# Optimization experiments

Hardware: AMD Instinct MI355X
Metric: run time of the kernel (lower is better)

The kernel has to match this reference:

```python
import jax, jax.numpy as jnp
import numpy as np

NUM_NODES = 10000  # fixed by input spec: edge_index values in [0, 10000)


def setup_inputs() -> dict:
    key = jax.random.key(0)
    k1, k2, k3 = jax.random.split(key, 3)
    N, E, D_IN, D_OUT = NUM_NODES, 320000, 256, 256
    x = jax.random.normal(k1, (N, D_IN), dtype=jnp.float32)
    edge_index = jax.random.randint(k2, (2, E), 0, N, dtype=jnp.int64)
    # ensure node N-1 appears so num_nodes == N as in the torch code
    edge_index = edge_index.at[0, 0].set(N - 1)
    # xavier_uniform for [D_IN, D_OUT]
    limit = float(np.sqrt(6.0 / (D_IN + D_OUT)))
    weight = jax.random.uniform(k3, (D_IN, D_OUT), dtype=jnp.float32,
                                minval=-limit, maxval=limit)
    return {"x": x, "edge_index": edge_index, "weight": weight}


def _normalize_adjacency(edge_index, num_nodes):
    src, dst = edge_index[0], edge_index[1]
    ones = jnp.ones(src.shape[0], dtype=jnp.float32)
    # symmetric binarized adjacency: adj[i,j] = adj[j,i] = 1 (set, not add)
    adj = jnp.zeros((num_nodes, num_nodes), dtype=jnp.float32)
    adj = adj.at[src, dst].max(ones)
    adj = adj.at[dst, src].max(ones)
    # one round of self-loops: adj += I
    adj = adj + jnp.eye(num_nodes, dtype=jnp.float32)
    deg = jnp.sum(adj, axis=1)                    # [N]
    dinv = 1.0 / jnp.sqrt(deg)                    # [N]
    # D^-1/2 A D^-1/2 via broadcasting (equivalent to diag mms)
    return adj * dinv[:, None] * dinv[None, :]


def reference(x, edge_index, weight):
    adj = _normalize_adjacency(edge_index, NUM_NODES)  # [N, N]
    h = adj @ x                                        # [N, D_IN]
    return h @ weight                                  # [N, D_OUT]
```

## Files before the change

### kernel.cpp

```cpp
#include <hip/hip_runtime.h>
#include <hip/hip_bf16.h>
#include <stdint.h>

#define N_NODES   10000
#define D_FEAT    256
#define E_EDGES   320000
#define ROW_WORDS 313
#define ROW_STRIDE 320
#define LIST_CAP  1024

#define NB     250
#define RPB    40
#define B_CAP  8192
#define NBLK_E 313
#define NBLK_W 64

typedef __attribute__((ext_vector_type(4))) float float4v;
typedef _Float16 half8  __attribute__((ext_vector_type(8)));
typedef _Float16 half4v __attribute__((ext_vector_type(4)));

__device__ __forceinline__ uint16_t f2bf(float f) {
    union { float f; uint32_t u; } v; v.f = f;
    uint32_t r = v.u + 0x7fffu + ((v.u >> 16) & 1u);
    return (uint16_t)(r >> 16);
}
__device__ __forceinline__ float lo16(uint32_t u) {
    union { uint32_t u; float f; } v; v.u = u << 16; return v.f;
}
__device__ __forceinline__ float hi16(uint32_t u) {
    union { uint32_t u; float f; } v; v.u = u & 0xffff0000u; return v.f;
}


__global__ void __launch_bounds__(1024)
fill_buckets(const int* __restrict__ ei, uint32_t* __restrict__ bucketbuf,
             uint32_t* __restrict__ cursors,
             const float* __restrict__ w, _Float16* __restrict__ wt) {
    __shared__ uint32_t hist[256];
    __shared__ uint32_t lofs[256];
    __shared__ uint32_t base_s[256];
    __shared__ uint32_t stage[2048];
    __shared__ uint16_t sbkt[2048];
    int t = threadIdx.x;

    if (blockIdx.x >= NBLK_E) {
        int kb = (blockIdx.x - NBLK_E) * 4;
        int k = kb + (t >> 8), n = t & 255;
        float* st = (float*)stage;
        st[(n << 2) | (t >> 8)] = w[(size_t)k * D_FEAT + n];
        __syncthreads();
        if (t < 256) {
            half4v o = { (_Float16)st[t * 4 + 0], (_Float16)st[t * 4 + 1],
                         (_Float16)st[t * 4 + 2], (_Float16)st[t * 4 + 3] };
            *(half4v*)&wt[(size_t)t * D_FEAT + kb] = o;
        }
        return;
    }

    if (t < 256) hist[t] = 0;
    __syncthreads();
    int e = blockIdx.x * 1024 + t;
    int b0 = -1, b1 = -1; uint32_t ent0 = 0, ent1 = 0, s0 = 0, s1 = 0;
    if (e < E_EDGES) {
        int s = ei[e], d = ei[E_EDGES + e];
        if ((uint32_t)s < N_NODES && (uint32_t)d < N_NODES) {
            b0 = s / RPB; ent0 = ((uint32_t)(s - b0 * RPB) << 14) | (uint32_t)d;
            b1 = d / RPB; ent1 = ((uint32_t)(d - b1 * RPB) << 14) | (uint32_t)s;
            s0 = atomicAdd(&hist[b0], 1u);
            s1 = atomicAdd(&hist[b1], 1u);
        }
    }
    __syncthreads();
    if (t < 256) lofs[t] = hist[t];
    __syncthreads();
    for (int d = 1; d < 256; d <<= 1) {
        uint32_t v = 0;
        if (t < 256 && t >= d) v = lofs[t - d];
        __syncthreads();
        if (t < 256) lofs[t] += v;
        __syncthreads();
    }
    if (t < 256) base_s[t] = hist[t] ? atomicAdd(&cursors[t], hist[t]) : 0u;
    if (b0 >= 0) {
        uint32_t p0 = lofs[b0] - hist[b0] + s0;
        stage[p0] = ent0; sbkt[p0] = (uint16_t)b0;
        uint32_t p1 = lofs[b1] - hist[b1] + s1;
        stage[p1] = ent1; sbkt[p1] = (uint16_t)b1;
    }
    __syncthreads();
    uint32_t total = lofs[255];
    for (uint32_t idx = t; idx < total; idx += 1024) {
        uint32_t b = sbkt[idx];
        uint32_t pos = base_s[b] + (idx - (lofs[b] - hist[b]));
        if (pos < B_CAP) bucketbuf[(size_t)b * B_CAP + pos] = stage[idx];
    }
}

__global__ void __launch_bounds__(1024)
bucket_to_csr(const uint32_t* __restrict__ bucketbuf,
              const uint32_t* __restrict__ cursors,
              uint32_t* __restrict__ gcursor,
              uint32_t* __restrict__ col, uint32_t* __restrict__ row_base,
              uint32_t* __restrict__ row_deg, float* __restrict__ dinv,
              const float* __restrict__ x, uint16_t* __restrict__ xs) {
    __shared__ uint32_t bm[RPB * ROW_WORDS];
    __shared__ uint32_t degs[RPB];
    __shared__ uint32_t rowoff[RPB];
    __shared__ uint32_t segbase;
    int b = blockIdx.x, t = threadIdx.x;
    for (int i = t; i < RPB * ROW_WORDS; i += 1024) bm[i] = 0;
    __syncthreads();
    uint32_t cnt = min(cursors[b], (uint32_t)B_CAP);
    const uint32_t* bb = bucketbuf + (size_t)b * B_CAP;
    for (uint32_t i = t; i < cnt; i += 1024) {
        uint32_t ent = bb[i];
        uint32_t lr = ent >> 14, d = ent & 0x3FFFu;
        atomicOr(&bm[lr * ROW_WORDS + (d >> 5)], 1u << (d & 31));
    }
    __syncthreads();
    int wv = t >> 6, lane = t & 63;
    for (int r = wv; r < RPB; r += 16) {
        int pop = 0;
        #pragma unroll
        for (int k = 0; k < 5; k++) {
            int w = lane + 64 * k;
            if (w < ROW_WORDS) pop += __popc(bm[r * ROW_WORDS + w]);
        }
        #pragma unroll
        for (int off = 32; off > 0; off >>= 1) pop += __shfl_xor(pop, off, 64);
        if (lane == 0) degs[r] = (uint32_t)pop;
    }
    __syncthreads();
    if (t == 0) {
        uint32_t run = 0;
        for (int r = 0; r < RPB; r++) {
            rowoff[r] = run;
            run += (degs[r] + 3u) & ~3u;
        }
        segbase = atomicAdd(gcursor, run);
    }
    __syncthreads();
    int row0 = b * RPB;
    for (int r = wv; r < RPB; r += 16) {
        int gi = row0 + r;
        uint32_t base = segbase + rowoff[r];
        float di = 1.0f / sqrtf((float)(degs[r] + 1u));
        if (lane == 0) {
            row_base[gi] = base;
            row_deg[gi]  = degs[r];
            dinv[gi]     = di;
        }
        float4v xv = *(const float4v*)(x + (size_t)gi * D_FEAT + lane * 4);
        uint2 o;
        o.x = (uint32_t)f2bf(di * xv[0]) | ((uint32_t)f2bf(di * xv[1]) << 16);
        o.y = (uint32_t)f2bf(di * xv[2]) | ((uint32_t)f2bf(di * xv[3]) << 16);
        *(uint2*)(xs + (size_t)gi * D_FEAT + lane * 4) = o;
        uint32_t wb[5]; int tot = 0;
        #pragma unroll
        for (int k = 0; k < 5; k++) {
            int w = lane + 64 * k;
            uint32_t v = (w < ROW_WORDS) ? bm[r * ROW_WORDS + w] : 0u;
            wb[k] = v; tot += __popc(v);
        }
        int incl = tot;
        #pragma unroll
        for (int off = 1; off < 64; off <<= 1) {
            int v = __shfl_up(incl, off, 64);
            if (lane >= off) incl += v;
        }
        uint32_t p = base + (uint32_t)(incl - tot);
        #pragma unroll
        for (int k = 0; k < 5; k++) {
            uint32_t bits = wb[k];
            uint32_t cbase = (uint32_t)(lane + 64 * k) << 5;
            while (bits) {
                col[p++] = cbase + (uint32_t)__builtin_ctz(bits);
                bits &= bits - 1;
            }
        }
    }
}

__global__ void __launch_bounds__(256)
spmm_csr(const uint32_t* __restrict__ row_base, const uint32_t* __restrict__ row_deg,
         const float* __restrict__ dinv, const uint32_t* __restrict__ col,
         const uint16_t* __restrict__ xs, _Float16* __restrict__ aggh) {
    int wv = threadIdx.x >> 6, lane = threadIdx.x & 63;
    int i = blockIdx.x * 4 + wv;
    uint32_t base = row_base[i], deg = row_deg[i];
    float di = dinv[i];
    float4v z = {0.f, 0.f, 0.f, 0.f};
    float4v acc0 = z, acc1 = z, acc2 = z, acc3 = z;
    size_t ch = (size_t)lane * 4;
    uint32_t t4 = deg & ~3u;
    for (uint32_t t = 0; t < t4; t += 4) {
        uint4 jv = *(const uint4*)&col[base + t];
        uint2 g0 = *(const uint2*)(xs + (size_t)jv.x * D_FEAT + ch);
        uint2 g1 = *(const uint2*)(xs + (size_t)jv.y * D_FEAT + ch);
        uint2 g2 = *(const uint2*)(xs + (size_t)jv.z * D_FEAT + ch);
        uint2 g3 = *(const uint2*)(xs + (size_t)jv.w * D_FEAT + ch);
        acc0[0] += lo16(g0.x); acc0[1] += hi16(g0.x); acc0[2] += lo16(g0.y); acc0[3] += hi16(g0.y);
        acc1[0] += lo16(g1.x); acc1[1] += hi16(g1.x); acc1[2] += lo16(g1.y); acc1[3] += hi16(g1.y);
        acc2[0] += lo16(g2.x); acc2[1] += hi16(g2.x); acc2[2] += lo16(g2.y); acc2[3] += hi16(g2.y);
        acc3[0] += lo16(g3.x); acc3[1] += hi16(g3.x); acc3[2] += lo16(g3.y); acc3[3] += hi16(g3.y);
    }
    for (uint32_t t = t4; t < deg; t++) {
        uint32_t j = col[base + t];
        uint2 g = *(const uint2*)(xs + (size_t)j * D_FEAT + ch);
        acc0[0] += lo16(g.x); acc0[1] += hi16(g.x); acc0[2] += lo16(g.y); acc0[3] += hi16(g.y);
    }
    uint2 gs = *(const uint2*)(xs + (size_t)i * D_FEAT + ch);
    acc1[0] += lo16(gs.x); acc1[1] += hi16(gs.x); acc1[2] += lo16(gs.y); acc1[3] += hi16(gs.y);
    float4v acc = (acc0 + acc1) + (acc2 + acc3);
    half4v o = { (_Float16)(di * acc[0]), (_Float16)(di * acc[1]),
                 (_Float16)(di * acc[2]), (_Float16)(di * acc[3]) };
    *(half4v*)(aggh + (size_t)i * D_FEAT + ch) = o;
}

__global__ void __launch_bounds__(256)
gemm_mfma(const _Float16* __restrict__ aggh, const _Float16* __restrict__ wt,
          float* __restrict__ out) {
    int t = threadIdx.x;
    int wv = t >> 6, lane = t & 63;
    int quad = lane >> 4, r = lane & 15;
    int bx = blockIdx.x;
    int ct = blockIdx.y * 4 + wv;

    const _Float16* pa = aggh + (size_t)(bx * 16 + r) * D_FEAT + quad * 8;
    const _Float16* pb = wt   + (size_t)(ct * 16 + r) * D_FEAT + quad * 8;

    float4v acc = {0.f, 0.f, 0.f, 0.f};
    #pragma unroll
    for (int kk = 0; kk < D_FEAT; kk += 32) {
        half8 a = *(const half8*)(pa + kk);
        half8 b = *(const half8*)(pb + kk);
        acc = __builtin_amdgcn_mfma_f32_16x16x32_f16(a, b, acc, 0, 0, 0);
    }
    int mbase = bx * 16 + quad * 4;
    int colg  = ct * 16 + r;
    #pragma unroll
    for (int u = 0; u < 4; u++)
        out[(size_t)(mbase + u) * D_FEAT + colg] = acc[u];
}


__global__ void scatter_edges_fb(const int* __restrict__ ei,
                                 uint32_t* __restrict__ bitmap) {
    int e = blockIdx.x * blockDim.x + threadIdx.x;
    if (e >= E_EDGES) return;
    int s = ei[e], d = ei[E_EDGES + e];
    if ((uint32_t)s >= N_NODES || (uint32_t)d >= N_NODES) return;
    atomicOr(&bitmap[(size_t)s * ROW_STRIDE + (d >> 5)], 1u << (d & 31));
    atomicOr(&bitmap[(size_t)d * ROW_STRIDE + (s >> 5)], 1u << (s & 31));
}

__global__ void __launch_bounds__(256)
popc_dinv(const uint32_t* __restrict__ bitmap, float* __restrict__ dinv) {
    int wv = threadIdx.x >> 6, lane = threadIdx.x & 63;
    int i = blockIdx.x * 4 + wv;
    const uint32_t* rb = bitmap + (size_t)i * ROW_STRIDE;
    int pop = 0;
    #pragma unroll
    for (int k = 0; k < 5; k++) {
        int w = lane + 64 * k;
        if (w < ROW_WORDS) pop += __popc(rb[w]);
    }
    #pragma unroll
    for (int off = 32; off > 0; off >>= 1) pop += __shfl_xor(pop, off, 64);
    if (lane == 0) dinv[i] = 1.0f / sqrtf((float)(pop + 1));
}

__global__ void __launch_bounds__(256)
spmm_bitmap_fb(const uint32_t* __restrict__ bitmap, const float* __restrict__ dinv,
               const float* __restrict__ xf, float* __restrict__ agg) {
    __shared__ __align__(16) uint32_t lists[4][LIST_CAP];
    int wv = threadIdx.x >> 6, lane = threadIdx.x & 63;
    int i = blockIdx.x * 4 + wv;
    uint32_t* list = lists[wv];
    const uint32_t* rb = bitmap + (size_t)i * ROW_STRIDE;

    uint32_t wbits[5]; int tot = 0;
    #pragma unroll
    for (int k = 0; k < 5; k++) {
        int w = lane + 64 * k;
        uint32_t b = (w < ROW_WORDS) ? rb[w] : 0u;
        wbits[k] = b;
        tot += __popc(b);
    }
    int incl = tot;
    #pragma unroll
    for (int off = 1; off < 64; off <<= 1) {
        int v = __shfl_up(incl, off, 64);
        if (lane >= off) incl += v;
    }
    uint32_t p = (uint32_t)(incl - tot);
    uint32_t deg = (uint32_t)__shfl(incl, 63, 64);
    #pragma unroll
    for (int k = 0; k < 5; k++) {
        uint32_t bits = wbits[k];
        uint32_t base = (uint32_t)(lane + 64 * k) << 5;
        while (bits) {
            if (p < LIST_CAP) list[p] = base + (uint32_t)__builtin_ctz(bits);
            p++;
            bits &= bits - 1;
        }
    }
    if (deg > LIST_CAP) deg = LIST_CAP;

    float di = dinv[i];
    float4v z = {0.f, 0.f, 0.f, 0.f};
    float4v acc0 = z, acc1 = z, acc2 = z, acc3 = z;
    float4v sv = *(const float4v*)(xf + (size_t)i * D_FEAT + lane * 4);
    uint32_t t4 = deg & ~3u;
    for (uint32_t k = 0; k < t4; k += 4) {
        uint4 jv = *(const uint4*)&list[k];
        float d0 = dinv[jv.x], d1 = dinv[jv.y], d2 = dinv[jv.z], d3 = dinv[jv.w];
        float4v v0 = *(const float4v*)(xf + (size_t)jv.x * D_FEAT + lane * 4);
        float4v v1 = *(const float4v*)(xf + (size_t)jv.y * D_FEAT + lane * 4);
        float4v v2 = *(const float4v*)(xf + (size_t)jv.z * D_FEAT + lane * 4);
        float4v v3 = *(const float4v*)(xf + (size_t)jv.w * D_FEAT + lane * 4);
        acc0 += d0 * v0; acc1 += d1 * v1; acc2 += d2 * v2; acc3 += d3 * v3;
    }
    for (uint32_t k = t4; k < deg; k++) {
        uint32_t j = list[k];
        acc0 += dinv[j] * (*(const float4v*)(xf + (size_t)j * D_FEAT + lane * 4));
    }
    float4v acc = (acc0 + acc1) + (acc2 + acc3) + di * sv;
    *(float4v*)(agg + (size_t)i * D_FEAT + lane * 4) = di * acc;
}

__global__ void __launch_bounds__(256)
gemm_valu(float* __restrict__ io, const float* __restrict__ wf) {
    __shared__ __align__(16) float a_lds[16 * D_FEAT];
    int c = threadIdx.x;
    int r0 = blockIdx.x * 16;
    for (int idx = c; idx < 16 * D_FEAT; idx += 256)
        a_lds[idx] = io[(size_t)r0 * D_FEAT + idx];
    __syncthreads();
    float acc[16];
    #pragma unroll
    for (int r = 0; r < 16; r++) acc[r] = 0.f;
    for (int k0 = 0; k0 < D_FEAT; k0 += 4) {
        float w0 = wf[(size_t)(k0 + 0) * D_FEAT + c];
        float w1 = wf[(size_t)(k0 + 1) * D_FEAT + c];
        float w2 = wf[(size_t)(k0 + 2) * D_FEAT + c];
        float w3 = wf[(size_t)(k0 + 3) * D_FEAT + c];
        #pragma unroll
        for (int r = 0; r < 16; r++) {
            float4v av = *(const float4v*)&a_lds[r * D_FEAT + k0];
            acc[r] = fmaf(av[3], w3, fmaf(av[2], w2,
                     fmaf(av[1], w1, fmaf(av[0], w0, acc[r]))));
        }
    }
    #pragma unroll
    for (int r = 0; r < 16; r++)
        io[(size_t)(r0 + r) * D_FEAT + c] = acc[r];
}

extern "C" void kernel_launch(void* const* d_in, const int* in_sizes, int n_in,
                              void* d_out, int out_size, void* d_ws, size_t ws_size,
                              hipStream_t stream) {
    const float* x  = (const float*)d_in[0];
    const int*   ei = (const int*)d_in[1];
    const float* w  = (const float*)d_in[2];
    float* out = (float*)d_out;
    uint8_t* ws = (uint8_t*)d_ws;

    const size_t CUR_OFF  = 8192000;
    const size_t RB_OFF   = 8194048;
    const size_t RD_OFF   = 8234048;
    const size_t DI_OFF   = 8274048;
    const size_t XS_OFF   = 8314048;
    const size_t COL_OFF  = 13434048;
    const size_t WT_OFF   = 16154048;
    const size_t NEED_NEW = 16285120;
    const size_t NEED_FB  = 12840000;

    if (ws_size >= NEED_NEW) {
        uint32_t* bucketbuf = (uint32_t*)ws;
        _Float16* aggh      = (_Float16*)ws;
        uint32_t* cursors   = (uint32_t*)(ws + CUR_OFF);
        uint32_t* row_base  = (uint32_t*)(ws + RB_OFF);
        uint32_t* row_deg   = (uint32_t*)(ws + RD_OFF);
        float*    dinv      = (float*)(ws + DI_OFF);
        uint16_t* xs        = (uint16_t*)(ws + XS_OFF);
        uint32_t* col       = (uint32_t*)(ws + COL_OFF);
        _Float16* wt        = (_Float16*)(ws + WT_OFF);

        hipMemsetAsync(cursors, 0, 2048, stream);
        fill_buckets <<<NBLK_E + NBLK_W, 1024, 0, stream>>>(ei, bucketbuf, cursors, w, wt);
        bucket_to_csr<<<NB, 1024, 0, stream>>>(bucketbuf, cursors, &cursors[NB],
                                               col, row_base, row_deg, dinv, x, xs);
        spmm_csr     <<<N_NODES / 4, 256, 0, stream>>>(row_base, row_deg, dinv, col, xs, aggh);
        gemm_mfma    <<<dim3(N_NODES / 16, 4), 256, 0, stream>>>(aggh, wt, out);
    } else if (ws_size >= NEED_FB) {
        uint32_t* bitmap = (uint32_t*)ws;
        float*    dinv   = (float*)(ws + 12800000);

        hipMemsetAsync(bitmap, 0, 12800000, stream);
        scatter_edges_fb<<<(E_EDGES + 255) / 256, 256, 0, stream>>>(ei, bitmap);
        popc_dinv      <<<N_NODES / 4, 256, 0, stream>>>(bitmap, dinv);
        spmm_bitmap_fb <<<N_NODES / 4, 256, 0, stream>>>(bitmap, dinv, x, out);
        gemm_valu      <<<N_NODES / 16, 256, 0, stream>>>(out, w);
    }
}
```

Before: 142.7 us.

## Split CSR build blocks, unroll SpMM gathers to 8, stage GEMM A tile in LDS

Three separate changes. The bucket-to-CSR kernel now launches two blocks per bucket, each handling half the rows, which doubles parallelism and halves the shared bitmap size, at the cost of every block reading the full bucket and filtering it. The SpMM inner loop is unrolled to 8 neighbour gathers with 8 accumulators, putting more loads in flight. The GEMM now has one block per 16-row strip load the A tile into padded LDS once and loop over 4 column tiles per wave, which cuts redundant global reads of A but gives the GEMM 4x fewer blocks.

```diff
diff --git a/kernel.cpp b/kernel.cpp
--- a/kernel.cpp
+++ b/kernel.cpp
@@ -14,6 +14,9 @@
 #define B_CAP  8192
 #define NBLK_E 313
 #define NBLK_W 64
+#define RPC    20
+
+#define LDSTR 264
 
 typedef __attribute__((ext_vector_type(4))) float float4v;
 typedef _Float16 half8  __attribute__((ext_vector_type(8)));
@@ -103,23 +106,28 @@
               uint32_t* __restrict__ col, uint32_t* __restrict__ row_base,
               uint32_t* __restrict__ row_deg, float* __restrict__ dinv,
               const float* __restrict__ x, uint16_t* __restrict__ xs) {
-    __shared__ uint32_t bm[RPB * ROW_WORDS];
-    __shared__ uint32_t degs[RPB];
-    __shared__ uint32_t rowoff[RPB];
+    __shared__ uint32_t bm[RPC * ROW_WORDS];
+    __shared__ uint32_t degs[RPC];
+    __shared__ uint32_t rowoff[RPC];
     __shared__ uint32_t segbase;
-    int b = blockIdx.x, t = threadIdx.x;
-    for (int i = t; i < RPB * ROW_WORDS; i += 1024) bm[i] = 0;
+    int blk = blockIdx.x, t = threadIdx.x;
+    int b   = blk >> 1;
+    int lr0 = (blk & 1) * RPC;
+    for (int i = t; i < RPC * ROW_WORDS; i += 1024) bm[i] = 0;
     __syncthreads();
     uint32_t cnt = min(cursors[b], (uint32_t)B_CAP);
     const uint32_t* bb = bucketbuf + (size_t)b * B_CAP;
     for (uint32_t i = t; i < cnt; i += 1024) {
         uint32_t ent = bb[i];
-        uint32_t lr = ent >> 14, d = ent & 0x3FFFu;
-        atomicOr(&bm[lr * ROW_WORDS + (d >> 5)], 1u << (d & 31));
+        uint32_t lr = (ent >> 14) - (uint32_t)lr0;
+        if (lr < RPC) {
+            uint32_t d = ent & 0x3FFFu;
+            atomicOr(&bm[lr * ROW_WORDS + (d >> 5)], 1u << (d & 31));
+        }
     }
     __syncthreads();
     int wv = t >> 6, lane = t & 63;
-    for (int r = wv; r < RPB; r += 16) {
+    for (int r = wv; r < RPC; r += 16) {
         int pop = 0;
         #pragma unroll
         for (int k = 0; k < 5; k++) {
@@ -133,15 +141,15 @@
     __syncthreads();
     if (t == 0) {
         uint32_t run = 0;
-        for (int r = 0; r < RPB; r++) {
+        for (int r = 0; r < RPC; r++) {
             rowoff[r] = run;
             run += (degs[r] + 3u) & ~3u;
         }
         segbase = atomicAdd(gcursor, run);
     }
     __syncthreads();
-    int row0 = b * RPB;
-    for (int r = wv; r < RPB; r += 16) {
+    int row0 = b * RPB + lr0;
+    for (int r = wv; r < RPC; r += 16) {
         int gi = row0 + r;
         uint32_t base = segbase + rowoff[r];
         float di = 1.0f / sqrtf((float)(degs[r] + 1u));
@@ -190,28 +198,38 @@
     uint32_t base = row_base[i], deg = row_deg[i];
     float di = dinv[i];
     float4v z = {0.f, 0.f, 0.f, 0.f};
-    float4v acc0 = z, acc1 = z, acc2 = z, acc3 = z;
+    float4v a0 = z, a1 = z, a2 = z, a3 = z, a4 = z, a5 = z, a6 = z, a7 = z;
     size_t ch = (size_t)lane * 4;
-    uint32_t t4 = deg & ~3u;
-    for (uint32_t t = 0; t < t4; t += 4) {
-        uint4 jv = *(const uint4*)&col[base + t];
-        uint2 g0 = *(const uint2*)(xs + (size_t)jv.x * D_FEAT + ch);
-        uint2 g1 = *(const uint2*)(xs + (size_t)jv.y * D_FEAT + ch);
-        uint2 g2 = *(const uint2*)(xs + (size_t)jv.z * D_FEAT + ch);
-        uint2 g3 = *(const uint2*)(xs + (size_t)jv.w * D_FEAT + ch);
-        acc0[0] += lo16(g0.x); acc0[1] += hi16(g0.x); acc0[2] += lo16(g0.y); acc0[3] += hi16(g0.y);
-        acc1[0] += lo16(g1.x); acc1[1] += hi16(g1.x); acc1[2] += lo16(g1.y); acc1[3] += hi16(g1.y);
-        acc2[0] += lo16(g2.x); acc2[1] += hi16(g2.x); acc2[2] += lo16(g2.y); acc2[3] += hi16(g2.y);
-        acc3[0] += lo16(g3.x); acc3[1] += hi16(g3.x); acc3[2] += lo16(g3.y); acc3[3] += hi16(g3.y);
-    }
-    for (uint32_t t = t4; t < deg; t++) {
+    uint32_t t8 = deg & ~7u;
+    uint32_t t = 0;
+    for (; t < t8; t += 8) {
+        uint4 jva = *(const uint4*)&col[base + t];
+        uint4 jvb = *(const uint4*)&col[base + t + 4];
+        uint2 g0 = *(const uint2*)(xs + (size_t)jva.x * D_FEAT + ch);
+        uint2 g1 = *(const uint2*)(xs + (size_t)jva.y * D_FEAT + ch);
+        uint2 g2 = *(const uint2*)(xs + (size_t)jva.z * D_FEAT + ch);
+        uint2 g3 = *(const uint2*)(xs + (size_t)jva.w * D_FEAT + ch);
+        uint2 g4 = *(const uint2*)(xs + (size_t)jvb.x * D_FEAT + ch);
+        uint2 g5 = *(const uint2*)(xs + (size_t)jvb.y * D_FEAT + ch);
+        uint2 g6 = *(const uint2*)(xs + (size_t)jvb.z * D_FEAT + ch);
+        uint2 g7 = *(const uint2*)(xs + (size_t)jvb.w * D_FEAT + ch);
+        a0[0] += lo16(g0.x); a0[1] += hi16(g0.x); a0[2] += lo16(g0.y); a0[3] += hi16(g0.y);
+        a1[0] += lo16(g1.x); a1[1] += hi16(g1.x); a1[2] += lo16(g1.y); a1[3] += hi16(g1.y);
+        a2[0] += lo16(g2.x); a2[1] += hi16(g2.x); a2[2] += lo16(g2.y); a2[3] += hi16(g2.y);
+        a3[0] += lo16(g3.x); a3[1] += hi16(g3.x); a3[2] += lo16(g3.y); a3[3] += hi16(g3.y);
+        a4[0] += lo16(g4.x); a4[1] += hi16(g4.x); a4[2] += lo16(g4.y); a4[3] += hi16(g4.y);
+        a5[0] += lo16(g5.x); a5[1] += hi16(g5.x); a5[2] += lo16(g5.y); a5[3] += hi16(g5.y);
+        a6[0] += lo16(g6.x); a6[1] += hi16(g6.x); a6[2] += lo16(g6.y); a6[3] += hi16(g6.y);
+        a7[0] += lo16(g7.x); a7[1] += hi16(g7.x); a7[2] += lo16(g7.y); a7[3] += hi16(g7.y);
+    }
+    for (; t < deg; t++) {
         uint32_t j = col[base + t];
         uint2 g = *(const uint2*)(xs + (size_t)j * D_FEAT + ch);
-        acc0[0] += lo16(g.x); acc0[1] += hi16(g.x); acc0[2] += lo16(g.y); acc0[3] += hi16(g.y);
+        a0[0] += lo16(g.x); a0[1] += hi16(g.x); a0[2] += lo16(g.y); a0[3] += hi16(g.y);
     }
     uint2 gs = *(const uint2*)(xs + (size_t)i * D_FEAT + ch);
-    acc1[0] += lo16(gs.x); acc1[1] += hi16(gs.x); acc1[2] += lo16(gs.y); acc1[3] += hi16(gs.y);
-    float4v acc = (acc0 + acc1) + (acc2 + acc3);
+    a1[0] += lo16(gs.x); a1[1] += hi16(gs.x); a1[2] += lo16(gs.y); a1[3] += hi16(gs.y);
+    float4v acc = ((a0 + a1) + (a2 + a3)) + ((a4 + a5) + (a6 + a7));
     half4v o = { (_Float16)(di * acc[0]), (_Float16)(di * acc[1]),
                  (_Float16)(di * acc[2]), (_Float16)(di * acc[3]) };
     *(half4v*)(aggh + (size_t)i * D_FEAT + ch) = o;
@@ -220,27 +238,33 @@
 __global__ void __launch_bounds__(256)
 gemm_mfma(const _Float16* __restrict__ aggh, const _Float16* __restrict__ wt,
           float* __restrict__ out) {
-    int t = threadIdx.x;
-    int wv = t >> 6, lane = t & 63;
+    __shared__ __align__(16) _Float16 a_lds[16 * LDSTR];
+    int t = threadIdx.x, wv = t >> 6, lane = t & 63;
+    int r0 = blockIdx.x * 16;
+    for (int idx = t * 8; idx < 16 * D_FEAT; idx += 256 * 8) {
+        int r = idx >> 8, c = idx & 255;
+        *(half8*)&a_lds[r * LDSTR + c] =
+            *(const half8*)&aggh[(size_t)(r0 + r) * D_FEAT + c];
+    }
+    __syncthreads();
     int quad = lane >> 4, r = lane & 15;
-    int bx = blockIdx.x;
-    int ct = blockIdx.y * 4 + wv;
-
-    const _Float16* pa = aggh + (size_t)(bx * 16 + r) * D_FEAT + quad * 8;
-    const _Float16* pb = wt   + (size_t)(ct * 16 + r) * D_FEAT + quad * 8;
-
-    float4v acc = {0.f, 0.f, 0.f, 0.f};
-    #pragma unroll
-    for (int kk = 0; kk < D_FEAT; kk += 32) {
-        half8 a = *(const half8*)(pa + kk);
-        half8 b = *(const half8*)(pb + kk);
-        acc = __builtin_amdgcn_mfma_f32_16x16x32_f16(a, b, acc, 0, 0, 0);
-    }
-    int mbase = bx * 16 + quad * 4;
-    int colg  = ct * 16 + r;
-    #pragma unroll
-    for (int u = 0; u < 4; u++)
-        out[(size_t)(mbase + u) * D_FEAT + colg] = acc[u];
+    int mbase = r0 + quad * 4;
+    #pragma unroll
+    for (int u = 0; u < 4; u++) {
+        int ct = wv * 4 + u;
+        const _Float16* pb = wt + (size_t)(ct * 16 + r) * D_FEAT + quad * 8;
+        float4v acc = {0.f, 0.f, 0.f, 0.f};
+        #pragma unroll
+        for (int kk = 0; kk < D_FEAT; kk += 32) {
+            half8 a = *(const half8*)&a_lds[r * LDSTR + kk + quad * 8];
+            half8 b = *(const half8*)(pb + kk);
+            acc = __builtin_amdgcn_mfma_f32_16x16x32_f16(a, b, acc, 0, 0, 0);
+        }
+        int colg = ct * 16 + r;
+        #pragma unroll
+        for (int v = 0; v < 4; v++)
+            out[(size_t)(mbase + v) * D_FEAT + colg] = acc[v];
+    }
 }
 
 
@@ -389,10 +413,10 @@
 
         hipMemsetAsync(cursors, 0, 2048, stream);
         fill_buckets <<<NBLK_E + NBLK_W, 1024, 0, stream>>>(ei, bucketbuf, cursors, w, wt);
-        bucket_to_csr<<<NB, 1024, 0, stream>>>(bucketbuf, cursors, &cursors[NB],
-                                               col, row_base, row_deg, dinv, x, xs);
+        bucket_to_csr<<<NB * 2, 1024, 0, stream>>>(bucketbuf, cursors, &cursors[NB],
+                                                   col, row_base, row_deg, dinv, x, xs);
         spmm_csr     <<<N_NODES / 4, 256, 0, stream>>>(row_base, row_deg, dinv, col, xs, aggh);
-        gemm_mfma    <<<dim3(N_NODES / 16, 4), 256, 0, stream>>>(aggh, wt, out);
+        gemm_mfma    <<<N_NODES / 16, 256, 0, stream>>>(aggh, wt, out);
     } else if (ws_size >= NEED_FB) {
         uint32_t* bitmap = (uint32_t*)ws;
         float*    dinv   = (float*)(ws + 12800000);
```

Measured after the change: 135.5 us. 1.05x faster.
